# Performance work log

Measured on AMD Instinct MI355X. Metric: run time of the kernel, lower is better.

Reference implementation:

```python
import jax, jax.numpy as jnp
import numpy as np

N_NODES = 81 * 4096   # 4096 graphs x 81 nodes (81 forced by h.view(-1,1,64*81))
N_EDGES = 4_000_000
HID = 32


def _edge_softmax(logits, mask, dst, n):
    # DGL edge_softmax restricted to masked edge subset, normalized per destination node
    NEG = jnp.float32(-1e30)
    l = jnp.where(mask, logits, NEG)
    m = jax.ops.segment_max(l, dst, num_segments=n)
    m = jnp.where(m > -1e29, m, 0.0)  # dst with no masked in-edges
    e = jnp.where(mask, jnp.exp(l - m[dst]), 0.0)
    s = jax.ops.segment_sum(e, dst, num_segments=n)
    return e / jnp.maximum(s[dst], 1e-20)


def _wsgconv(h, src, dst, w, n, W, b, bias, cs, cp, cn):
    pos = w > 0
    neg = w < 0
    a_p = _edge_softmax(w, pos, dst, n)            # softmax of w on positive subgraph
    a_n = _edge_softmax(jnp.abs(w), neg, dst, n)   # softmax of |w| on negative subgraph
    h_p = jax.ops.segment_sum(h[src] * a_p[:, None], dst, num_segments=n)
    h_n = jax.ops.segment_sum(h[src] * a_n[:, None], dst, num_segments=n)
    comb = jnp.concatenate([cs * h, cp * h_p, cn * h_n], axis=1)
    return jax.nn.relu(comb @ W.T + b + bias)


def _conv1d(x, k, stride):
    return jax.lax.conv_general_dilated(x, k, (stride,), 'VALID',
                                        dimension_numbers=('NCH', 'OIH', 'NCH'))


def reference(src, dst, w, n_nodes, W1, b1, bias1, c1s, c1p, c1n,
              W2, b2, bias2, c2s, c2p, c2n, k1, bk1, k2, bk2, Wfc, bfc, Wc, bc):
    n = n_nodes
    deg = jax.ops.segment_sum(jnp.ones_like(w), dst, num_segments=n)
    h0 = deg[:, None]                                  # in_degrees feature [N,1]
    h1 = _wsgconv(h0, src, dst, w, n, W1, b1, bias1, c1s, c1p, c1n)
    h2 = _wsgconv(h1, src, dst, w, n, W2, b2, bias2, c2s, c2p, c2n)
    h = jnp.concatenate([h1, h2], axis=1)              # JumpingKnowledge('cat') -> [N,64]
    # GSAPool(ratio=1.0) returns the input feature unchanged -> identity
    B = n // 81
    x = h.reshape(B, 1, 64 * 81)
    x = _conv1d(x, k1, 64) + bk1[None, :, None]        # [B,16,81]
    x = x[..., :80].reshape(B, 16, 40, 2).max(-1)      # MaxPool1d(2) -> [B,16,40]
    x = _conv1d(x, k2, 3) + bk2[None, :, None]         # [B,32,13]
    x = x.reshape(B, 32 * 13)
    x = jax.nn.relu(x @ Wfc.T + bfc)
    # F.dropout skipped (deterministic reference)
    logits = x @ Wc.T + bc
    return jax.nn.log_softmax(logits, axis=-1)


def setup_inputs():
    key = jax.random.key(0)
    ks = jax.random.split(key, 16)
    s = 0.1
    return {
        'src': jax.random.randint(ks[0], (N_EDGES,), 0, N_NODES),
        'dst': jax.random.randint(ks[1], (N_EDGES,), 0, N_NODES),
        'w': jax.random.normal(ks[2], (N_EDGES,), jnp.float32),
        'n_nodes': N_NODES,
        'W1': jax.random.normal(ks[3], (HID, 3), jnp.float32) * s,
        'b1': jax.random.normal(ks[4], (HID,), jnp.float32) * s,
        'bias1': jnp.zeros((HID,), jnp.float32),
        'c1s': jnp.ones((1,), jnp.float32),
        'c1p': jnp.ones((1,), jnp.float32),
        'c1n': jnp.ones((1,), jnp.float32),
        'W2': jax.random.normal(ks[5], (HID, 3 * HID), jnp.float32) * s,
        'b2': jax.random.normal(ks[6], (HID,), jnp.float32) * s,
        'bias2': jnp.zeros((HID,), jnp.float32),
        'c2s': jnp.ones((1,), jnp.float32),
        'c2p': jnp.ones((1,), jnp.float32),
        'c2n': jnp.ones((1,), jnp.float32),
        'k1': jax.random.normal(ks[7], (16, 1, 64), jnp.float32) * s,
        'bk1': jax.random.normal(ks[8], (16,), jnp.float32) * s,
        'k2': jax.random.normal(ks[9], (32, 16, 3), jnp.float32) * s,
        'bk2': jax.random.normal(ks[10], (32,), jnp.float32) * s,
        'Wfc': jax.random.normal(ks[11], (128, 32 * 13), jnp.float32) * s,
        'bfc': jax.random.normal(ks[12], (128,), jnp.float32) * s,
        'Wc': jax.random.normal(ks[13], (10, 128), jnp.float32) * s,
        'bc': jax.random.normal(ks[14], (10,), jnp.float32) * s,
    }
```

## Files before the change

kernel.cpp:

```cpp
#include <hip/hip_runtime.h>
#include <hip/hip_bf16.h>

#define NNODES 331776
#define NGRAPH 4096
#define NBUCK  2048
#define BNODES 162
#define TE     4096
#define CAP    2560
#define CH     64
#define EB     16

typedef __attribute__((ext_vector_type(8))) short bf8;
typedef __attribute__((ext_vector_type(4))) float f4;
typedef __attribute__((ext_vector_type(4))) unsigned int u32x4;

static __device__ __forceinline__ short f2bf(float x) {
    return (short)__builtin_bit_cast(unsigned short, __float2bfloat16(x));
}
static __device__ __forceinline__ float bf2f(unsigned short u) {
    return __bfloat162float(__hip_bfloat16_raw{u});
}


__global__ __launch_bounds__(256) void k_hist(const int* __restrict__ dst,
                                              int* __restrict__ H, int E) {
    __shared__ int h[NBUCK];
    int t = threadIdx.x, b = blockIdx.x;
    for (int i = t; i < NBUCK; i += 256) h[i] = 0;
    __syncthreads();
    int lo = b * TE;
    int bins[EB]; bool ok[EB];
#pragma unroll
    for (int i = 0; i < EB; i++) {
        int e = lo + i * 256 + t;
        ok[i] = e < E;
        bins[i] = ok[i] ? (dst[e] / BNODES) : 0;
    }
#pragma unroll
    for (int i = 0; i < EB; i++)
        if (ok[i]) atomicAdd(&h[bins[i]], 1);
    __syncthreads();
    for (int i = t; i < NBUCK; i += 256) H[b * NBUCK + i] = h[i];
}

__global__ __launch_bounds__(256) void k_colA(const int* __restrict__ H,
                                              int* __restrict__ P,
                                              int NT, int CS) {
    int idx = blockIdx.x * 256 + threadIdx.x;
    int bin = idx & (NBUCK - 1);
    int chunk = idx >> 11;
    int t0 = chunk * CS, t1 = min(NT, t0 + CS);
    int s = 0;
    for (int t = t0; t < t1; t++) s += H[t * NBUCK + bin];
    P[chunk * NBUCK + bin] = s;
}

__global__ __launch_bounds__(256) void k_colB(int* __restrict__ P,
                                              int* __restrict__ T) {
    int bin = blockIdx.x * 256 + threadIdx.x;
    int s = 0;
    for (int c = 0; c < CH; c++) {
        int v = P[c * NBUCK + bin];
        P[c * NBUCK + bin] = s;
        s += v;
    }
    T[bin] = s;
}

__global__ __launch_bounds__(256) void k_colC(int* __restrict__ H,
                                              const int* __restrict__ P,
                                              int NT, int CS) {
    int idx = blockIdx.x * 256 + threadIdx.x;
    int bin = idx & (NBUCK - 1);
    int chunk = idx >> 11;
    int t0 = chunk * CS, t1 = min(NT, t0 + CS);
    int s = P[chunk * NBUCK + bin];
    for (int t = t0; t < t1; t++) {
        int v = H[t * NBUCK + bin];
        H[t * NBUCK + bin] = s;
        s += v;
    }
}

__global__ __launch_bounds__(256) void k_binscan(const int* __restrict__ T,
                                                 int* __restrict__ Bstart) {
    __shared__ int tmp[256];
    int t = threadIdx.x;
    int base = t * 8;
    int loc[8]; int s = 0;
#pragma unroll
    for (int i = 0; i < 8; i++) { loc[i] = s; s += T[base + i]; }
    tmp[t] = s; __syncthreads();
    for (int o = 1; o < 256; o <<= 1) {
        int a = (t >= o) ? tmp[t - o] : 0;
        __syncthreads();
        tmp[t] += a;
        __syncthreads();
    }
    int excl = tmp[t] - s;
#pragma unroll
    for (int i = 0; i < 8; i++) Bstart[base + i] = excl + loc[i];
    if (t == 255) Bstart[NBUCK] = excl + s;
}

__global__ __launch_bounds__(256) void k_place(
    const int* __restrict__ src, const int* __restrict__ dst,
    const float* __restrict__ w,
    const int* __restrict__ H, const int* __restrict__ Bstart,
    int2* __restrict__ csrB, int E) {
    __shared__ int cur[NBUCK];
    int t = threadIdx.x, b = blockIdx.x;
    for (int i = t; i < NBUCK; i += 256)
        cur[i] = Bstart[i] + H[b * NBUCK + i];
    __syncthreads();
    int lo = b * TE;
    int dd[EB], sx[EB]; float wv[EB]; bool ok[EB];
#pragma unroll
    for (int i = 0; i < EB; i++) {
        int e = lo + i * 256 + t;
        ok[i] = e < E;
        if (ok[i]) { dd[i] = dst[e]; sx[i] = src[e]; wv[i] = w[e]; }
    }
    int pk0[EB]; float es[EB]; int bin[EB];
#pragma unroll
    for (int i = 0; i < EB; i++) {
        if (ok[i]) {
            float v = wv[i];
            float e2 = 0.f;
            if (v > 0.f)      e2 = __expf(v);
            else if (v < 0.f) e2 = -__expf(-v);
            es[i] = e2;
            bin[i] = dd[i] / BNODES;
            pk0[i] = sx[i] | ((dd[i] - bin[i] * BNODES) << 19);
        }
    }
    int p[EB];
#pragma unroll
    for (int i = 0; i < EB; i++)
        if (ok[i]) p[i] = atomicAdd(&cur[bin[i]], 1);
#pragma unroll
    for (int i = 0; i < EB; i++)
        if (ok[i]) {
            int2 pk;
            pk.x = pk0[i];
            pk.y = __float_as_int(es[i]);
            csrB[p[i]] = pk;
        }
}

__global__ __launch_bounds__(256) void k_sortbucket(
    int2* __restrict__ csrB, const int* __restrict__ Bstart,
    int* __restrict__ cnt, int* __restrict__ cntp, int* __restrict__ offs) {
    __shared__ int2 pb[CAP];
    __shared__ int lcnt[BNODES * 2];
    __shared__ int lpos[BNODES * 2];
    int t = threadIdx.x, b = blockIdx.x;
    int lo = Bstart[b];
    int S  = Bstart[b + 1] - lo;
    if (S > CAP) S = CAP;
    for (int i = t; i < BNODES * 2; i += 256) lcnt[i] = 0;
    __syncthreads();
    for (int i = t; i < S; i += 256) {
        int2 pk = csrB[lo + i];
        pb[i] = pk;
        int key = ((pk.x >> 19) << 1) | ((unsigned)pk.y >> 31);
        atomicAdd(&lcnt[key], 1);
    }
    __syncthreads();
    if (t == 0) {
        int s = 0;
        for (int i = 0; i < BNODES * 2; i++) { lpos[i] = s; s += lcnt[i]; }
    }
    __syncthreads();
    int node0 = b * BNODES;
    for (int i = t; i < BNODES; i += 256) {
        cnt[node0 + i]  = lcnt[2 * i] + lcnt[2 * i + 1];
        cntp[node0 + i] = lcnt[2 * i];
        offs[node0 + i] = lo + lpos[2 * i];
    }
    __syncthreads();
    for (int i = t; i < S; i += 256) {
        int2 pk = pb[i];
        int local = pk.x >> 19;
        int sign  = (unsigned)pk.y >> 31;
        int key = (local << 1) | sign;
        int p = atomicAdd(&lpos[key], 1);
        int d7 = (node0 + local) & 7;
        int2 outv;
        outv.x = (pk.x & 0x7FFFF) | (d7 << 19) | (sign << 22);
        outv.y = pk.y & 0x7FFFFFFF;
        csrB[lo + p] = outv;
    }
}


__global__ __launch_bounds__(256) void k_layer1(
    const int* __restrict__ cnt, const int* __restrict__ cntp,
    const int* __restrict__ offs, const int2* __restrict__ csr,
    float* __restrict__ spos, float* __restrict__ sneg,
    unsigned short* __restrict__ h1b,
    unsigned long long* __restrict__ xtab,
    const float* __restrict__ W1, const float* __restrict__ b1,
    const float* __restrict__ bias1,
    const float* __restrict__ c1s, const float* __restrict__ c1p,
    const float* __restrict__ c1n) {
    int t = threadIdx.x;
    int g = t >> 5, f = t & 31;
    int d = blockIdx.x * 8 + g;
    int beg = offs[d];
    int len = cnt[d];
    int np  = cntp[d];
    float sp = 0.f, sn = 0.f, up = 0.f, un = 0.f;
    for (int j = 0; j < len; j += 32) {
        int rem = len - j;
        if (f < rem) {
            int2 sw = csr[beg + j + f];
            float es = __int_as_float(sw.y);
            float degs = (float)cnt[sw.x & 0x7FFFF];
            float ep = (j + f < np) ? es : 0.f;
            float en = es - ep;
            sp += ep; sn += en;
            up = fmaf(degs, ep, up); un = fmaf(degs, en, un);
        }
    }
    for (int m = 16; m; m >>= 1) {
        sp += __shfl_xor(sp, m, 32);
        sn += __shfl_xor(sn, m, 32);
        up += __shfl_xor(up, m, 32);
        un += __shfl_xor(un, m, 32);
    }
    if (f == 0) { spos[d] = sp; sneg[d] = sn; }
    float hp = up / fmaxf(sp, 1e-20f);
    float hn = un / fmaxf(sn, 1e-20f);
    float x0 = c1s[0] * (float)len;
    float x1 = c1p[0] * hp;
    float x2 = c1n[0] * hn;
    if (f == 0) {
        unsigned long long u0 = (unsigned short)f2bf(x0);
        unsigned long long u1 = (unsigned short)f2bf(x1);
        unsigned long long u2 = (unsigned short)f2bf(x2);
        xtab[d] = u0 | (u1 << 16) | (u2 << 32) | (0x3F80ULL << 48);
    }
    float v = W1[f * 3] * x0 + W1[f * 3 + 1] * x1 + W1[f * 3 + 2] * x2
            + b1[f] + bias1[f];
    v = fmaxf(v, 0.f);
    h1b[d * 32 + f] = (unsigned short)f2bf(v);
}


__global__ __launch_bounds__(256) void k_agg(
    const int* __restrict__ cnt, const int* __restrict__ offs,
    const int2* __restrict__ csr,
    const float* __restrict__ spos, const float* __restrict__ sneg,
    const unsigned long long* __restrict__ xtab,
    const unsigned short* __restrict__ W1Tb,
    unsigned short* __restrict__ hpb, unsigned short* __restrict__ hnb,
    int E) {
    __shared__ unsigned short Hl[4][32][40];
    int t = threadIdx.x;
    int wv = t >> 6, lane = t & 63;
    int col = lane & 15, quad = lane >> 4;
    int d0 = (blockIdx.x * 4 + wv) * 8;
    int beg = offs[d0];
    int totlen = 0;
#pragma unroll
    for (int i = 0; i < 8; i++) totlen += cnt[d0 + i];

    bf8 B1[2];
#pragma unroll
    for (int fh = 0; fh < 2; fh++) {
        u32x4 bw = {0u, 0u, 0u, 0u};
        if (quad == 0) {
            int n = fh * 16 + col;
            unsigned w0 = W1Tb[0 * 32 + n], w1 = W1Tb[1 * 32 + n];
            unsigned w2 = W1Tb[2 * 32 + n], w3 = W1Tb[3 * 32 + n];
            bw.x = w0 | (w1 << 16);
            bw.y = w2 | (w3 << 16);
        }
        B1[fh] = __builtin_bit_cast(bf8, bw);
    }

    f4 acc2[2] = {{0.f, 0.f, 0.f, 0.f}, {0.f, 0.f, 0.f, 0.f}};
    unsigned short (*myH)[40] = Hl[wv];
    int nw = (totlen + 31) >> 5;

    for (int w = 0; w < nw; w++) {
        int eidx = w * 32 + (lane & 31);
        bool val = eidx < totlen;
        int gidx = beg + (val ? eidx : 0);
        long long rec = *(const long long*)(csr + gidx);
        int x = (int)rec;
        float ef = __int_as_float((int)(rec >> 32));
        int slot = val ? (((x >> 19) & 7) * 2 + ((x >> 22) & 1)) : 255;
        unsigned es16 = (unsigned)(unsigned short)f2bf(ef);
        int pk = (int)(es16 | ((unsigned)slot << 16));

#pragma unroll
        for (int eh = 0; eh < 2; eh++) {
            int xm = __builtin_amdgcn_ds_bpermute((eh * 16 + col) * 4, x);
            unsigned srcn = (unsigned)xm & 0x7FFFF;
            unsigned long long r8 = 0;
            if (quad == 0) r8 = xtab[srcn];
            u32x4 av = {(unsigned)r8, (unsigned)(r8 >> 32), 0u, 0u};
            bf8 A1 = __builtin_bit_cast(bf8, av);
#pragma unroll
            for (int fh = 0; fh < 2; fh++) {
                f4 h = {0.f, 0.f, 0.f, 0.f};
                h = __builtin_amdgcn_mfma_f32_16x16x32_bf16(A1, B1[fh], h, 0, 0, 0);
#pragma unroll
                for (int i = 0; i < 4; i += 2) {
                    float lo = fmaxf(h[i], 0.f), hi = fmaxf(h[i + 1], 0.f);
                    unsigned u;
                    asm("v_cvt_pk_bf16_f32 %0, %1, %2" : "=v"(u) : "v"(lo), "v"(hi));
                    *(unsigned*)&myH[fh * 16 + col][eh * 16 + quad * 4 + i] = u;
                }
            }
        }

        unsigned aw[4];
#pragma unroll
        for (int j2 = 0; j2 < 4; j2++) {
            int k0 = quad * 8 + j2 * 2;
            int p0 = __builtin_amdgcn_ds_bpermute(k0 * 4, pk);
            int p1 = __builtin_amdgcn_ds_bpermute((k0 + 1) * 4, pk);
            unsigned e0 = (((unsigned)p0 >> 16) == (unsigned)col)
                        ? ((unsigned)p0 & 0xFFFFu) : 0u;
            unsigned e1 = (((unsigned)p1 >> 16) == (unsigned)col)
                        ? ((unsigned)p1 & 0xFFFFu) : 0u;
            aw[j2] = e0 | (e1 << 16);
        }
        bf8 A2 = __builtin_bit_cast(bf8, (u32x4){aw[0], aw[1], aw[2], aw[3]});

#pragma unroll
        for (int fh = 0; fh < 2; fh++) {
            bf8 B2 = *(const bf8*)&myH[fh * 16 + col][quad * 8];
            acc2[fh] = __builtin_amdgcn_mfma_f32_16x16x32_bf16(A2, B2, acc2[fh], 0, 0, 0);
        }
    }

#pragma unroll
    for (int i = 0; i < 4; i++) {
        int slot = quad * 4 + i;
        int node = d0 + (slot >> 1);
        float s = (slot & 1) ? sneg[node] : spos[node];
        float r = 1.0f / fmaxf(s, 1e-20f);
        unsigned short* bp = (slot & 1) ? hnb : hpb;
#pragma unroll
        for (int fh = 0; fh < 2; fh++) {
            float v = acc2[fh][i] * r;
            bp[(size_t)node * 32 + fh * 16 + col] = (unsigned short)f2bf(v);
        }
    }
}


__global__ __launch_bounds__(256) void k_prep(
    const float* __restrict__ W2, const float* __restrict__ c2s,
    const float* __restrict__ c2p, const float* __restrict__ c2n,
    const float* __restrict__ k1,
    const float* __restrict__ W1, const float* __restrict__ b1,
    const float* __restrict__ bias1,
    unsigned short* __restrict__ W2sT, unsigned short* __restrict__ k1T,
    unsigned short* __restrict__ W1Tb) {
    int i = blockIdx.x * 256 + threadIdx.x;
    if (i < 96 * 32) {
        int k = i >> 5, n = i & 31;
        float sc = (k < 32) ? c2s[0] : ((k < 64) ? c2p[0] : c2n[0]);
        W2sT[i] = (unsigned short)f2bf(W2[n * 96 + k] * sc);
    } else if (i < 96 * 32 + 64 * 16) {
        int j = i - 3072;
        int k = j >> 4, o = j & 15;
        k1T[j] = (unsigned short)f2bf(k1[o * 64 + k]);
    } else if (i < 96 * 32 + 64 * 16 + 4 * 32) {
        int j = i - (3072 + 1024);
        int k = j >> 5, n = j & 31;
        float v = (k < 3) ? W1[n * 3 + k] : (b1[n] + bias1[n]);
        W1Tb[j] = (unsigned short)f2bf(v);
    }
}


__global__ __launch_bounds__(256) void k_mlp_mfma(
    const unsigned short* __restrict__ h1b,
    const unsigned short* __restrict__ hpb, const unsigned short* __restrict__ hnb,
    const unsigned short* __restrict__ W2sT, const unsigned short* __restrict__ k1T,
    const float* __restrict__ b2, const float* __restrict__ bias2,
    const float* __restrict__ bk1,
    float* __restrict__ y1) {
    __shared__ unsigned short h2s[4][16 * 32];
    int t = threadIdx.x;
    int wv = t >> 6;
    int lane = t & 63;
    int col = lane & 15;
    int quad = lane >> 4;

    float bv0 = b2[col] + bias2[col];
    float bv1 = b2[col + 16] + bias2[col + 16];
    float bky = bk1[col];

    bf8 BW[2][3];
#pragma unroll
    for (int nt = 0; nt < 2; nt++)
#pragma unroll
        for (int kt = 0; kt < 3; kt++) {
            bf8 b;
#pragma unroll
            for (int j = 0; j < 8; j++)
                b[j] = (short)W2sT[(kt * 32 + quad * 8 + j) * 32 + nt * 16 + col];
            BW[nt][kt] = b;
        }
    bf8 BK[2];
#pragma unroll
    for (int kt = 0; kt < 2; kt++) {
        bf8 b;
#pragma unroll
        for (int j = 0; j < 8; j++)
            b[j] = (short)k1T[(kt * 32 + quad * 8 + j) * 16 + col];
        BK[kt] = b;
    }
    unsigned short* myT = h2s[wv];

#pragma unroll 1
    for (int g = 0; g < 4; g++) {
        int nbase = blockIdx.x * 256 + wv * 64 + g * 16;
        int node = nbase + col;
        bf8 a0 = *(const bf8*)(h1b + (size_t)node * 32 + quad * 8);
        bf8 a1 = *(const bf8*)(hpb + (size_t)node * 32 + quad * 8);
        bf8 a2 = *(const bf8*)(hnb + (size_t)node * 32 + quad * 8);

        f4 acc0 = {bv0, bv0, bv0, bv0};
        f4 acc1 = {bv1, bv1, bv1, bv1};
        acc0 = __builtin_amdgcn_mfma_f32_16x16x32_bf16(a0, BW[0][0], acc0, 0, 0, 0);
        acc0 = __builtin_amdgcn_mfma_f32_16x16x32_bf16(a1, BW[0][1], acc0, 0, 0, 0);
        acc0 = __builtin_amdgcn_mfma_f32_16x16x32_bf16(a2, BW[0][2], acc0, 0, 0, 0);
        acc1 = __builtin_amdgcn_mfma_f32_16x16x32_bf16(a0, BW[1][0], acc1, 0, 0, 0);
        acc1 = __builtin_amdgcn_mfma_f32_16x16x32_bf16(a1, BW[1][1], acc1, 0, 0, 0);
        acc1 = __builtin_amdgcn_mfma_f32_16x16x32_bf16(a2, BW[1][2], acc1, 0, 0, 0);

#pragma unroll
        for (int i = 0; i < 4; i++) {
            int r = quad * 4 + i;
            myT[r * 32 + col]      = (unsigned short)f2bf(fmaxf(acc0[i], 0.f));
            myT[r * 32 + col + 16] = (unsigned short)f2bf(fmaxf(acc1[i], 0.f));
        }
        bf8 ah2 = *(const bf8*)(myT + col * 32 + quad * 8);

        f4 accy = {bky, bky, bky, bky};
        accy = __builtin_amdgcn_mfma_f32_16x16x32_bf16(a0,  BK[0], accy, 0, 0, 0);
        accy = __builtin_amdgcn_mfma_f32_16x16x32_bf16(ah2, BK[1], accy, 0, 0, 0);
#pragma unroll
        for (int i = 0; i < 4; i++)
            y1[(size_t)(nbase + quad * 4 + i) * 16 + col] = accy[i];
    }
}


__global__ void k_transpose(const float* __restrict__ Wfc, float* __restrict__ WfcT) {
    int i = blockIdx.x * 256 + threadIdx.x;
    if (i < 128 * 416) {
        int u = i / 416, c = i - u * 416;
        WfcT[c * 128 + u] = Wfc[i];
    }
}


__global__ __launch_bounds__(128) void k_head(
    const float* __restrict__ y1, const float* __restrict__ k2,
    const float* __restrict__ bk2, const float* __restrict__ WfcT,
    const float* __restrict__ bfc, const float* __restrict__ Wc,
    const float* __restrict__ bc, float* __restrict__ out) {
    __shared__ float yl[1296];
    __shared__ float zl[16][41];
    __shared__ float xr[416];
    __shared__ float k2s[1536];
    __shared__ float fl[128];
    __shared__ float ll[10];
    int t = threadIdx.x;
    int b = blockIdx.x;
    const float* yb = y1 + (size_t)b * 1296;
    for (int i = t; i < 1296; i += 128) yl[i] = yb[i];
    for (int i = t; i < 1536; i += 128) k2s[i] = k2[i];
    __syncthreads();
    for (int i = t; i < 640; i += 128) {
        int ic = i & 15, p = i >> 4;
        zl[ic][p] = fmaxf(yl[(2 * p) * 16 + ic], yl[(2 * p + 1) * 16 + ic]);
    }
    __syncthreads();
    for (int i = t; i < 416; i += 128) {
        int oc = i / 13, tt = i - oc * 13;
        float acc = bk2[oc];
        for (int ic = 0; ic < 16; ic++) {
            const float* kk = &k2s[(oc * 16 + ic) * 3];
            acc += zl[ic][3 * tt]     * kk[0]
                 + zl[ic][3 * tt + 1] * kk[1]
                 + zl[ic][3 * tt + 2] * kk[2];
        }
        xr[i] = acc;
    }
    __syncthreads();
    {
        float acc = bfc[t];
        for (int i = 0; i < 416; i++) acc += xr[i] * WfcT[i * 128 + t];
        fl[t] = fmaxf(acc, 0.f);
    }
    __syncthreads();
    if (t < 10) {
        float acc = bc[t];
        for (int u = 0; u < 128; u++) acc += fl[u] * Wc[t * 128 + u];
        ll[t] = acc;
    }
    __syncthreads();
    if (t < 10) {
        float m = -1e30f;
        for (int c = 0; c < 10; c++) m = fmaxf(m, ll[c]);
        float s = 0.f;
        for (int c = 0; c < 10; c++) s += __expf(ll[c] - m);
        out[b * 10 + t] = ll[t] - m - __logf(s);
    }
}


extern "C" void kernel_launch(void* const* d_in, const int* in_sizes, int n_in,
                              void* d_out, int out_size, void* d_ws, size_t ws_size,
                              hipStream_t stream) {
    const int*   src   = (const int*)d_in[0];
    const int*   dst   = (const int*)d_in[1];
    const float* w     = (const float*)d_in[2];
    const float* W1    = (const float*)d_in[4];
    const float* b1    = (const float*)d_in[5];
    const float* bias1 = (const float*)d_in[6];
    const float* c1s   = (const float*)d_in[7];
    const float* c1p   = (const float*)d_in[8];
    const float* c1n   = (const float*)d_in[9];
    const float* W2    = (const float*)d_in[10];
    const float* b2    = (const float*)d_in[11];
    const float* bias2 = (const float*)d_in[12];
    const float* c2s   = (const float*)d_in[13];
    const float* c2p   = (const float*)d_in[14];
    const float* c2n   = (const float*)d_in[15];
    const float* k1    = (const float*)d_in[16];
    const float* bk1   = (const float*)d_in[17];
    const float* k2    = (const float*)d_in[18];
    const float* bk2   = (const float*)d_in[19];
    const float* Wfc   = (const float*)d_in[20];
    const float* bfc   = (const float*)d_in[21];
    const float* Wc    = (const float*)d_in[22];
    const float* bc    = (const float*)d_in[23];
    const int E = in_sizes[0];
    const int NT = (E + TE - 1) / TE;
    const int CS = (NT + CH - 1) / CH;

    size_t off = 0;
    auto carve = [&](size_t bytes) -> char* {
        char* p = (char*)d_ws + off;
        off = (off + bytes + 255) & ~(size_t)255;
        return p;
    };
    int*   cnt    = (int*)  carve((size_t)NNODES * 4);
    int*   cntp   = (int*)  carve((size_t)NNODES * 4);
    int*   offs   = (int*)  carve((size_t)NNODES * 4);
    int2*  csrB   = (int2*) carve((size_t)E * 8);
    int*   H      = (int*)  carve((size_t)NT * NBUCK * 4);
    int*   P      = (int*)  carve((size_t)CH * NBUCK * 4);
    int*   T      = (int*)  carve((size_t)NBUCK * 4);
    int*   Bstart = (int*)  carve((size_t)(NBUCK + 1) * 4);
    float* spos   = (float*)carve((size_t)NNODES * 4);
    float* sneg   = (float*)carve((size_t)NNODES * 4);
    unsigned short* h1b = (unsigned short*)carve((size_t)NNODES * 32 * 2);
    unsigned short* hpb = (unsigned short*)carve((size_t)NNODES * 32 * 2);
    unsigned short* hnb = (unsigned short*)carve((size_t)NNODES * 32 * 2);
    float* y1     = (float*)carve((size_t)NNODES * 16 * 4);
    float* WfcT   = (float*)carve((size_t)128 * 416 * 4);
    unsigned short* W2sT = (unsigned short*)carve((size_t)96 * 32 * 2);
    unsigned short* k1T  = (unsigned short*)carve((size_t)64 * 16 * 2);
    unsigned short* W1Tb = (unsigned short*)carve((size_t)4 * 32 * 2);
    unsigned long long* xtab = (unsigned long long*)y1;
    (void)ws_size;

    k_hist      <<<NT, 256, 0, stream>>>(dst, H, E);
    k_colA      <<<CH * NBUCK / 256, 256, 0, stream>>>(H, P, NT, CS);
    k_colB      <<<NBUCK / 256, 256, 0, stream>>>(P, T);
    k_colC      <<<CH * NBUCK / 256, 256, 0, stream>>>(H, P, NT, CS);
    k_binscan   <<<1, 256, 0, stream>>>(T, Bstart);
    k_place     <<<NT, 256, 0, stream>>>(src, dst, w, H, Bstart, csrB, E);
    k_sortbucket<<<NBUCK, 256, 0, stream>>>(csrB, Bstart, cnt, cntp, offs);
    k_layer1    <<<NNODES / 8, 256, 0, stream>>>(cnt, cntp, offs, csrB,
                                                 spos, sneg, h1b, xtab,
                                                 W1, b1, bias1, c1s, c1p, c1n);
    k_prep      <<<17, 256, 0, stream>>>(W2, c2s, c2p, c2n, k1,
                                         W1, b1, bias1, W2sT, k1T, W1Tb);
    k_transpose <<<(128 * 416 + 255) / 256, 256, 0, stream>>>(Wfc, WfcT);
    k_agg       <<<NNODES / 32, 256, 0, stream>>>(cnt, offs, csrB,
                                                  spos, sneg, xtab, W1Tb,
                                                  hpb, hnb, E);
    k_mlp_mfma  <<<NNODES / 256, 256, 0, stream>>>(h1b, hpb, hnb, W2sT, k1T,
                                                   b2, bias2, bk1, y1);
    k_head      <<<NGRAPH, 128, 0, stream>>>(y1, k2, bk2, WfcT, bfc, Wc, bc,
                                             (float*)d_out);
}
```

Baseline: 402.8 us.

## Batch four graphs per head block with shared FC weights; enlarge edge tiles

The head kernel now processes four graphs per block with 256 threads. It stages the transposed FC weight matrix in shared memory in two 64-column halves and reuses it across all four graphs, splits the 416-long dot products across four thread groups, and computes the classifier with shuffle reductions. Separately, the histogram and placement kernels each handle four times more edges per block through an inner pass loop, which cuts the number of per-block histogram rows. The goal is to cut repeated global weight reads and the column-scan work. The cost is large shared memory use per head block, which lowers occupancy, plus extra syncs. NT must be derived from TE in the hidden launch code for the larger edge tiles to stay correct.

```diff
diff --git a/kernel.cpp b/kernel.cpp
--- a/kernel.cpp
+++ b/kernel.cpp
@@ -5,10 +5,12 @@
 #define NGRAPH 4096
 #define NBUCK  2048
 #define BNODES 162
-#define TE     4096
+#define TE     16384
+#define PASSES 4
 #define CAP    2560
 #define CH     64
 #define EB     16
+#define HG     4
 
 typedef __attribute__((ext_vector_type(8))) short bf8;
 typedef __attribute__((ext_vector_type(4))) float f4;
@@ -28,17 +30,19 @@
     int t = threadIdx.x, b = blockIdx.x;
     for (int i = t; i < NBUCK; i += 256) h[i] = 0;
     __syncthreads();
-    int lo = b * TE;
-    int bins[EB]; bool ok[EB];
-#pragma unroll
-    for (int i = 0; i < EB; i++) {
-        int e = lo + i * 256 + t;
-        ok[i] = e < E;
-        bins[i] = ok[i] ? (dst[e] / BNODES) : 0;
-    }
-#pragma unroll
-    for (int i = 0; i < EB; i++)
-        if (ok[i]) atomicAdd(&h[bins[i]], 1);
+    for (int pass = 0; pass < PASSES; pass++) {
+        int lo = b * TE + pass * (EB * 256);
+        int bins[EB]; bool ok[EB];
+#pragma unroll
+        for (int i = 0; i < EB; i++) {
+            int e = lo + i * 256 + t;
+            ok[i] = e < E;
+            bins[i] = ok[i] ? (dst[e] / BNODES) : 0;
+        }
+#pragma unroll
+        for (int i = 0; i < EB; i++)
+            if (ok[i]) atomicAdd(&h[bins[i]], 1);
+    }
     __syncthreads();
     for (int i = t; i < NBUCK; i += 256) H[b * NBUCK + i] = h[i];
 }
@@ -113,39 +117,41 @@
     for (int i = t; i < NBUCK; i += 256)
         cur[i] = Bstart[i] + H[b * NBUCK + i];
     __syncthreads();
-    int lo = b * TE;
-    int dd[EB], sx[EB]; float wv[EB]; bool ok[EB];
-#pragma unroll
-    for (int i = 0; i < EB; i++) {
-        int e = lo + i * 256 + t;
-        ok[i] = e < E;
-        if (ok[i]) { dd[i] = dst[e]; sx[i] = src[e]; wv[i] = w[e]; }
-    }
-    int pk0[EB]; float es[EB]; int bin[EB];
-#pragma unroll
-    for (int i = 0; i < EB; i++) {
-        if (ok[i]) {
-            float v = wv[i];
-            float e2 = 0.f;
-            if (v > 0.f)      e2 = __expf(v);
-            else if (v < 0.f) e2 = -__expf(-v);
-            es[i] = e2;
-            bin[i] = dd[i] / BNODES;
-            pk0[i] = sx[i] | ((dd[i] - bin[i] * BNODES) << 19);
-        }
-    }
-    int p[EB];
-#pragma unroll
-    for (int i = 0; i < EB; i++)
-        if (ok[i]) p[i] = atomicAdd(&cur[bin[i]], 1);
-#pragma unroll
-    for (int i = 0; i < EB; i++)
-        if (ok[i]) {
-            int2 pk;
-            pk.x = pk0[i];
-            pk.y = __float_as_int(es[i]);
-            csrB[p[i]] = pk;
-        }
+    for (int pass = 0; pass < PASSES; pass++) {
+        int lo = b * TE + pass * (EB * 256);
+        int dd[EB], sx[EB]; float wv[EB]; bool ok[EB];
+#pragma unroll
+        for (int i = 0; i < EB; i++) {
+            int e = lo + i * 256 + t;
+            ok[i] = e < E;
+            if (ok[i]) { dd[i] = dst[e]; sx[i] = src[e]; wv[i] = w[e]; }
+        }
+        int pk0[EB]; float es[EB]; int bin[EB];
+#pragma unroll
+        for (int i = 0; i < EB; i++) {
+            if (ok[i]) {
+                float v = wv[i];
+                float e2 = 0.f;
+                if (v > 0.f)      e2 = __expf(v);
+                else if (v < 0.f) e2 = -__expf(-v);
+                es[i] = e2;
+                bin[i] = dd[i] / BNODES;
+                pk0[i] = sx[i] | ((dd[i] - bin[i] * BNODES) << 19);
+            }
+        }
+        int p[EB];
+#pragma unroll
+        for (int i = 0; i < EB; i++)
+            if (ok[i]) p[i] = atomicAdd(&cur[bin[i]], 1);
+#pragma unroll
+        for (int i = 0; i < EB; i++)
+            if (ok[i]) {
+                int2 pk;
+                pk.x = pk0[i];
+                pk.y = __float_as_int(es[i]);
+                csrB[p[i]] = pk;
+            }
+    }
 }
 
 __global__ __launch_bounds__(256) void k_sortbucket(
@@ -464,58 +470,86 @@
 }
 
 
-__global__ __launch_bounds__(128) void k_head(
+__global__ __launch_bounds__(256) void k_head(
     const float* __restrict__ y1, const float* __restrict__ k2,
     const float* __restrict__ bk2, const float* __restrict__ WfcT,
     const float* __restrict__ bfc, const float* __restrict__ Wc,
     const float* __restrict__ bc, float* __restrict__ out) {
+    __shared__ float wfc_l[416 * 64];
+    __shared__ float xr_all[HG][416];
+    __shared__ float fl_all[HG][128];
     __shared__ float yl[1296];
     __shared__ float zl[16][41];
-    __shared__ float xr[416];
     __shared__ float k2s[1536];
-    __shared__ float fl[128];
-    __shared__ float ll[10];
+    __shared__ float fl2[256];
+    __shared__ float ll[HG][10];
     int t = threadIdx.x;
-    int b = blockIdx.x;
-    const float* yb = y1 + (size_t)b * 1296;
-    for (int i = t; i < 1296; i += 128) yl[i] = yb[i];
-    for (int i = t; i < 1536; i += 128) k2s[i] = k2[i];
-    __syncthreads();
-    for (int i = t; i < 640; i += 128) {
-        int ic = i & 15, p = i >> 4;
-        zl[ic][p] = fmaxf(yl[(2 * p) * 16 + ic], yl[(2 * p + 1) * 16 + ic]);
-    }
-    __syncthreads();
-    for (int i = t; i < 416; i += 128) {
-        int oc = i / 13, tt = i - oc * 13;
-        float acc = bk2[oc];
-        for (int ic = 0; ic < 16; ic++) {
-            const float* kk = &k2s[(oc * 16 + ic) * 3];
-            acc += zl[ic][3 * tt]     * kk[0]
-                 + zl[ic][3 * tt + 1] * kk[1]
-                 + zl[ic][3 * tt + 2] * kk[2];
-        }
-        xr[i] = acc;
-    }
-    __syncthreads();
-    {
-        float acc = bfc[t];
-        for (int i = 0; i < 416; i++) acc += xr[i] * WfcT[i * 128 + t];
-        fl[t] = fmaxf(acc, 0.f);
-    }
-    __syncthreads();
-    if (t < 10) {
-        float acc = bc[t];
-        for (int u = 0; u < 128; u++) acc += fl[u] * Wc[t * 128 + u];
-        ll[t] = acc;
-    }
-    __syncthreads();
-    if (t < 10) {
+    int b0 = blockIdx.x * HG;
+    for (int i = t; i < 1536; i += 256) k2s[i] = k2[i];
+    for (int g = 0; g < HG; g++) {
+        const float4* yb4 = (const float4*)(y1 + (size_t)(b0 + g) * 1296);
+        __syncthreads();
+        for (int i = t; i < 324; i += 256) ((float4*)yl)[i] = yb4[i];
+        __syncthreads();
+        for (int i = t; i < 640; i += 256) {
+            int ic = i & 15, p = i >> 4;
+            zl[ic][p] = fmaxf(yl[(2 * p) * 16 + ic], yl[(2 * p + 1) * 16 + ic]);
+        }
+        __syncthreads();
+        for (int i = t; i < 416; i += 256) {
+            int oc = i / 13, tt = i - oc * 13;
+            float acc = bk2[oc];
+            for (int ic = 0; ic < 16; ic++) {
+                const float* kk = &k2s[(oc * 16 + ic) * 3];
+                acc += zl[ic][3 * tt]     * kk[0]
+                     + zl[ic][3 * tt + 1] * kk[1]
+                     + zl[ic][3 * tt + 2] * kk[2];
+            }
+            xr_all[g][i] = acc;
+        }
+    }
+    for (int uo = 0; uo < 2; uo++) {
+        __syncthreads();
+        for (int i = t; i < 416 * 64; i += 256) {
+            int r = i >> 6, u = i & 63;
+            wfc_l[i] = WfcT[r * 128 + uo * 64 + u];
+        }
+        __syncthreads();
+        int q = t >> 6, u = t & 63;
+        for (int g = 0; g < HG; g++) {
+            float acc = 0.f;
+            const float* xr = xr_all[g];
+            for (int i = q * 104; i < q * 104 + 104; i++)
+                acc = fmaf(xr[i], wfc_l[i * 64 + u], acc);
+            fl2[t] = acc;
+            __syncthreads();
+            if (t < 64)
+                fl_all[g][uo * 64 + t] =
+                    fmaxf(fl2[t] + fl2[64 + t] + fl2[128 + t] + fl2[192 + t]
+                          + bfc[uo * 64 + t], 0.f);
+            __syncthreads();
+        }
+    }
+    if (t < 160) {
+        int c = t >> 4, l = t & 15;
+        for (int g = 0; g < HG; g++) {
+            float acc = 0.f;
+            const float* fl = fl_all[g];
+            for (int i = l * 8; i < l * 8 + 8; i++)
+                acc += fl[i] * Wc[c * 128 + i];
+            for (int m = 8; m; m >>= 1) acc += __shfl_down(acc, m, 16);
+            if (l == 0) ll[g][c] = acc + bc[c];
+        }
+    }
+    __syncthreads();
+    if (t < HG * 10) {
+        int g = t / 10, c = t - g * 10;
+        const float* lg = ll[g];
         float m = -1e30f;
-        for (int c = 0; c < 10; c++) m = fmaxf(m, ll[c]);
+        for (int k = 0; k < 10; k++) m = fmaxf(m, lg[k]);
         float s = 0.f;
-        for (int c = 0; c < 10; c++) s += __expf(ll[c] - m);
-        out[b * 10 + t] = ll[t] - m - __logf(s);
+        for (int k = 0; k < 10; k++) s += __expf(lg[k] - m);
+        out[(b0 + g) * 10 + c] = lg[c] - m - __logf(s);
     }
 }
 
@@ -595,6 +629,6 @@
                                                   hpb, hnb, E);
     k_mlp_mfma  <<<NNODES / 256, 256, 0, stream>>>(h1b, hpb, hnb, W2sT, k1T,
                                                    b2, bias2, bk1, y1);
-    k_head      <<<NGRAPH, 128, 0, stream>>>(y1, k2, bk2, WfcT, bfc, Wc, bc,
-                                             (float*)d_out);
-}
+    k_head      <<<NGRAPH / HG, 256, 0, stream>>>(y1, k2, bk2, WfcT, bfc, Wc, bc,
+                                                  (float*)d_out);
+}
```

Measured after the change: 466.5 us. 1.16x slower.

## Coarsen histogram/place blocks and widen head kernel to 256 threads

Applied to the files above, without the earlier changes.

Each histogram and placement block now handles four times as many edges across several passes. This cuts the number of per-block histogram rows that the column-scan kernels must reduce, and the cost of clearing and writing the 2048-bin shared histogram each block. The head kernel moves to 256 threads: the FC reduction is split across two thread halves, the classifier dot products use a 16-lane shuffle reduction, and y1 is loaded with float4. The trade-off is fewer blocks, and so less parallelism, in the edge-bucketing kernels.

```diff
diff --git a/kernel.cpp b/kernel.cpp
--- a/kernel.cpp
+++ b/kernel.cpp
@@ -5,7 +5,8 @@
 #define NGRAPH 4096
 #define NBUCK  2048
 #define BNODES 162
-#define TE     4096
+#define TE     16384
+#define PASSES 4
 #define CAP    2560
 #define CH     64
 #define EB     16
@@ -28,17 +29,19 @@
     int t = threadIdx.x, b = blockIdx.x;
     for (int i = t; i < NBUCK; i += 256) h[i] = 0;
     __syncthreads();
-    int lo = b * TE;
-    int bins[EB]; bool ok[EB];
-#pragma unroll
-    for (int i = 0; i < EB; i++) {
-        int e = lo + i * 256 + t;
-        ok[i] = e < E;
-        bins[i] = ok[i] ? (dst[e] / BNODES) : 0;
-    }
-#pragma unroll
-    for (int i = 0; i < EB; i++)
-        if (ok[i]) atomicAdd(&h[bins[i]], 1);
+    for (int pass = 0; pass < PASSES; pass++) {
+        int lo = b * TE + pass * (EB * 256);
+        int bins[EB]; bool ok[EB];
+#pragma unroll
+        for (int i = 0; i < EB; i++) {
+            int e = lo + i * 256 + t;
+            ok[i] = e < E;
+            bins[i] = ok[i] ? (dst[e] / BNODES) : 0;
+        }
+#pragma unroll
+        for (int i = 0; i < EB; i++)
+            if (ok[i]) atomicAdd(&h[bins[i]], 1);
+    }
     __syncthreads();
     for (int i = t; i < NBUCK; i += 256) H[b * NBUCK + i] = h[i];
 }
@@ -113,39 +116,41 @@
     for (int i = t; i < NBUCK; i += 256)
         cur[i] = Bstart[i] + H[b * NBUCK + i];
     __syncthreads();
-    int lo = b * TE;
-    int dd[EB], sx[EB]; float wv[EB]; bool ok[EB];
-#pragma unroll
-    for (int i = 0; i < EB; i++) {
-        int e = lo + i * 256 + t;
-        ok[i] = e < E;
-        if (ok[i]) { dd[i] = dst[e]; sx[i] = src[e]; wv[i] = w[e]; }
-    }
-    int pk0[EB]; float es[EB]; int bin[EB];
-#pragma unroll
-    for (int i = 0; i < EB; i++) {
-        if (ok[i]) {
-            float v = wv[i];
-            float e2 = 0.f;
-            if (v > 0.f)      e2 = __expf(v);
-            else if (v < 0.f) e2 = -__expf(-v);
-            es[i] = e2;
-            bin[i] = dd[i] / BNODES;
-            pk0[i] = sx[i] | ((dd[i] - bin[i] * BNODES) << 19);
-        }
-    }
-    int p[EB];
-#pragma unroll
-    for (int i = 0; i < EB; i++)
-        if (ok[i]) p[i] = atomicAdd(&cur[bin[i]], 1);
-#pragma unroll
-    for (int i = 0; i < EB; i++)
-        if (ok[i]) {
-            int2 pk;
-            pk.x = pk0[i];
-            pk.y = __float_as_int(es[i]);
-            csrB[p[i]] = pk;
-        }
+    for (int pass = 0; pass < PASSES; pass++) {
+        int lo = b * TE + pass * (EB * 256);
+        int dd[EB], sx[EB]; float wv[EB]; bool ok[EB];
+#pragma unroll
+        for (int i = 0; i < EB; i++) {
+            int e = lo + i * 256 + t;
+            ok[i] = e < E;
+            if (ok[i]) { dd[i] = dst[e]; sx[i] = src[e]; wv[i] = w[e]; }
+        }
+        int pk0[EB]; float es[EB]; int bin[EB];
+#pragma unroll
+        for (int i = 0; i < EB; i++) {
+            if (ok[i]) {
+                float v = wv[i];
+                float e2 = 0.f;
+                if (v > 0.f)      e2 = __expf(v);
+                else if (v < 0.f) e2 = -__expf(-v);
+                es[i] = e2;
+                bin[i] = dd[i] / BNODES;
+                pk0[i] = sx[i] | ((dd[i] - bin[i] * BNODES) << 19);
+            }
+        }
+        int p[EB];
+#pragma unroll
+        for (int i = 0; i < EB; i++)
+            if (ok[i]) p[i] = atomicAdd(&cur[bin[i]], 1);
+#pragma unroll
+        for (int i = 0; i < EB; i++)
+            if (ok[i]) {
+                int2 pk;
+                pk.x = pk0[i];
+                pk.y = __float_as_int(es[i]);
+                csrB[p[i]] = pk;
+            }
+    }
 }
 
 __global__ __launch_bounds__(256) void k_sortbucket(
@@ -464,7 +469,7 @@
 }
 
 
-__global__ __launch_bounds__(128) void k_head(
+__global__ __launch_bounds__(256) void k_head(
     const float* __restrict__ y1, const float* __restrict__ k2,
     const float* __restrict__ bk2, const float* __restrict__ WfcT,
     const float* __restrict__ bfc, const float* __restrict__ Wc,
@@ -473,20 +478,21 @@
     __shared__ float zl[16][41];
     __shared__ float xr[416];
     __shared__ float k2s[1536];
+    __shared__ float fl2[256];
     __shared__ float fl[128];
     __shared__ float ll[10];
     int t = threadIdx.x;
     int b = blockIdx.x;
-    const float* yb = y1 + (size_t)b * 1296;
-    for (int i = t; i < 1296; i += 128) yl[i] = yb[i];
-    for (int i = t; i < 1536; i += 128) k2s[i] = k2[i];
-    __syncthreads();
-    for (int i = t; i < 640; i += 128) {
+    const float4* yb4 = (const float4*)(y1 + (size_t)b * 1296);
+    for (int i = t; i < 324; i += 256) ((float4*)yl)[i] = yb4[i];
+    for (int i = t; i < 1536; i += 256) k2s[i] = k2[i];
+    __syncthreads();
+    for (int i = t; i < 640; i += 256) {
         int ic = i & 15, p = i >> 4;
         zl[ic][p] = fmaxf(yl[(2 * p) * 16 + ic], yl[(2 * p + 1) * 16 + ic]);
     }
     __syncthreads();
-    for (int i = t; i < 416; i += 128) {
+    for (int i = t; i < 416; i += 256) {
         int oc = i / 13, tt = i - oc * 13;
         float acc = bk2[oc];
         for (int ic = 0; ic < 16; ic++) {
@@ -499,15 +505,23 @@
     }
     __syncthreads();
     {
-        float acc = bfc[t];
-        for (int i = 0; i < 416; i++) acc += xr[i] * WfcT[i * 128 + t];
-        fl[t] = fmaxf(acc, 0.f);
-    }
-    __syncthreads();
-    if (t < 10) {
-        float acc = bc[t];
-        for (int u = 0; u < 128; u++) acc += fl[u] * Wc[t * 128 + u];
-        ll[t] = acc;
+        int u = t & 127, q = t >> 7;
+        float acc = 0.f;
+        for (int i = q * 208; i < q * 208 + 208; i++)
+            acc = fmaf(xr[i], WfcT[i * 128 + u], acc);
+        fl2[t] = acc;
+    }
+    __syncthreads();
+    if (t < 128)
+        fl[t] = fmaxf(fl2[t] + fl2[t + 128] + bfc[t], 0.f);
+    __syncthreads();
+    if (t < 160) {
+        int c = t >> 4, l = t & 15;
+        float acc = 0.f;
+        for (int i = l * 8; i < l * 8 + 8; i++)
+            acc += fl[i] * Wc[c * 128 + i];
+        for (int m = 8; m; m >>= 1) acc += __shfl_down(acc, m, 16);
+        if (l == 0) ll[c] = acc + bc[c];
     }
     __syncthreads();
     if (t < 10) {
@@ -595,6 +609,6 @@
                                                   hpb, hnb, E);
     k_mlp_mfma  <<<NNODES / 256, 256, 0, stream>>>(h1b, hpb, hnb, W2sT, k1T,
                                                    b2, bias2, bk1, y1);
-    k_head      <<<NGRAPH, 128, 0, stream>>>(y1, k2, bk2, WfcT, bfc, Wc, bc,
+    k_head      <<<NGRAPH, 256, 0, stream>>>(y1, k2, bk2, WfcT, bfc, Wc, bc,
                                              (float*)d_out);
 }
```

After: 402.6 us. Within noise of the previous version (-0.0%).
